# Performance work log

Hardware: AMD Instinct MI355X
Metric: run time of the kernel (lower is better)

Reference implementation:

```python
import jax, jax.numpy as jnp
import numpy as np

D_IN = 1024
D_OUT = 1024
NUM_HEADS = 16
HEAD_DIM = D_OUT // NUM_HEADS


def setup_inputs() -> dict:
    key = jax.random.key(0)
    k = jax.random.split(key, 6)
    s = 1.0 / np.sqrt(D_IN)
    return {
        "x": jax.random.normal(k[0], (2, 2048, D_IN), dtype=jnp.float32),
        "W_q": jax.random.uniform(k[1], (D_OUT, D_IN), jnp.float32, -s, s),
        "W_k": jax.random.uniform(k[2], (D_OUT, D_IN), jnp.float32, -s, s),
        "W_v": jax.random.uniform(k[3], (D_OUT, D_IN), jnp.float32, -s, s),
        "W_o": jax.random.uniform(k[4], (D_OUT, D_OUT), jnp.float32, -s, s),
        "b_o": jax.random.uniform(k[5], (D_OUT,), jnp.float32, -s, s),
    }


def reference(x, W_q, W_k, W_v, W_o, b_o):
    b, n, _ = x.shape
    h, hd = NUM_HEADS, HEAD_DIM
    # linear projections (torch Linear: x @ W.T), reshape to [b, h, n, hd]
    q = (x @ W_q.T).reshape(b, n, h, hd).transpose(0, 2, 1, 3)
    k = (x @ W_k.T).reshape(b, n, h, hd).transpose(0, 2, 1, 3)
    v = (x @ W_v.T).reshape(b, n, h, hd).transpose(0, 2, 1, 3)
    scores = jnp.einsum("bhqd,bhkd->bhqk", q, k) / np.sqrt(hd).astype(np.float32)
    causal = jnp.triu(jnp.full((n, n), -jnp.inf, dtype=scores.dtype), k=1)
    scores = scores + causal[None, None]
    weights = jax.nn.softmax(scores, axis=-1)  # dropout p=0.0 -> identity
    ctx = jnp.einsum("bhqk,bhkd->bhqd", weights, v)
    ctx = ctx.transpose(0, 2, 1, 3).reshape(b, n, h * hd)
    return ctx @ W_o.T + b_o
```

## Files before the change

### kernel.cpp

```cpp
#include <hip/hip_runtime.h>
#include <hip/hip_bf16.h>
#include <stdint.h>

typedef __attribute__((ext_vector_type(8)))  __bf16   bf16x8;
typedef __attribute__((ext_vector_type(4)))  float    f32x4;
typedef __attribute__((ext_vector_type(16))) float    f32x16;
typedef __attribute__((ext_vector_type(4)))  unsigned u32x4;
typedef __attribute__((ext_vector_type(2)))  unsigned u32x2;

#define BATCH  2
#define SEQ    2048
#define DMODEL 1024
#define NHEAD  16
#define HDIM   64
#define MTOT   (BATCH * SEQ)
#define MOFF   8.0f

__device__ __forceinline__ void gload_lds16(const void* g, void* l) {
  __builtin_amdgcn_global_load_lds(
      (const __attribute__((address_space(1))) unsigned int*)g,
      (__attribute__((address_space(3))) unsigned int*)(uintptr_t)l,
      16, 0, 0);
}

__device__ __forceinline__ unsigned pkbf(float a, float b) {
  unsigned lo = (unsigned)__builtin_bit_cast(unsigned short, (__bf16)a);
  unsigned hb = (unsigned)__builtin_bit_cast(unsigned short, (__bf16)b);
  return lo | (hb << 16);
}

__global__ void cast_all(const float* __restrict__ x,  const float* __restrict__ wq,
                         const float* __restrict__ wk, const float* __restrict__ wv,
                         const float* __restrict__ wo,
                         __bf16* __restrict__ xb,  __bf16* __restrict__ wqb,
                         __bf16* __restrict__ wkb, __bf16* __restrict__ wvb,
                         __bf16* __restrict__ wob)
{
  const float* in; __bf16* out; int n;
  switch (blockIdx.y) {
    case 0:  in = x;  out = xb;  n = MTOT * DMODEL;   break;
    case 1:  in = wq; out = wqb; n = DMODEL * DMODEL; break;
    case 2:  in = wk; out = wkb; n = DMODEL * DMODEL; break;
    case 3:  in = wv; out = wvb; n = DMODEL * DMODEL; break;
    default: in = wo; out = wob; n = DMODEL * DMODEL; break;
  }
  const int i = blockIdx.x * blockDim.x + threadIdx.x;
  const int stride = gridDim.x * blockDim.x;
  for (int idx = i; idx * 8 < n; idx += stride) {
    const float4 a = ((const float4*)in)[idx * 2];
    const float4 b = ((const float4*)in)[idx * 2 + 1];
    bf16x8 v = { (__bf16)a.x, (__bf16)a.y, (__bf16)a.z, (__bf16)a.w,
                 (__bf16)b.x, (__bf16)b.y, (__bf16)b.z, (__bf16)b.w };
    *(bf16x8*)(out + (size_t)idx * 8) = v;
  }
}

__device__ __forceinline__ void gemm_tile_128(const __bf16* __restrict__ A,
                                              const __bf16* __restrict__ W,
                                              int bm, int bn, int Kd,
                                              f32x4 (&acc)[4][4])
{
  __shared__ __align__(16) __bf16 As[128 * 32];
  __shared__ __align__(16) __bf16 Bs[128 * 32];
  const int tid  = threadIdx.x;
  const int wave = tid >> 6, lane = tid & 63;
  const int wr = wave >> 1, wc = wave & 1;
  const int fr = lane & 15, fq = lane >> 4;
  const int c0 = tid, c1 = tid + 256;
  const __bf16* gA0 = A + (size_t)(bm * 128 + (c0 >> 2)) * Kd + (c0 & 3) * 8;
  const __bf16* gA1 = A + (size_t)(bm * 128 + (c1 >> 2)) * Kd + (c1 & 3) * 8;
  const __bf16* gB0 = W + (size_t)(bn * 128 + (c0 >> 2)) * Kd + (c0 & 3) * 8;
  const __bf16* gB1 = W + (size_t)(bn * 128 + (c1 >> 2)) * Kd + (c1 & 3) * 8;

  for (int k0 = 0; k0 < Kd; k0 += 32) {
    gload_lds16(gA0 + k0, As + c0 * 8);
    gload_lds16(gB0 + k0, Bs + c0 * 8);
    gload_lds16(gA1 + k0, As + c1 * 8);
    gload_lds16(gB1 + k0, Bs + c1 * 8);
    __syncthreads();
    bf16x8 a[4], b[4];
#pragma unroll
    for (int m = 0; m < 4; ++m)
      a[m] = *(const bf16x8*)(As + (wr * 64 + m * 16 + fr) * 32 + fq * 8);
#pragma unroll
    for (int n = 0; n < 4; ++n)
      b[n] = *(const bf16x8*)(Bs + (wc * 64 + n * 16 + fr) * 32 + fq * 8);
#pragma unroll
    for (int m = 0; m < 4; ++m)
#pragma unroll
      for (int n = 0; n < 4; ++n)
        acc[m][n] = __builtin_amdgcn_mfma_f32_16x16x32_bf16(a[m], b[n], acc[m][n], 0, 0, 0);
    __syncthreads();
  }
}

__global__ __launch_bounds__(256)
void gemm_qkv(const __bf16* __restrict__ xb,
              const __bf16* __restrict__ Wq, const __bf16* __restrict__ Wk,
              const __bf16* __restrict__ Wv,
              __bf16* __restrict__ Qo, __bf16* __restrict__ Ko, __bf16* __restrict__ VTo,
              float qscale)
{
  const int z = blockIdx.z;
  const __bf16* A; const __bf16* W; __bf16* Ob; int bm, bn;
  if (z == 2)      { A = Wv; W = xb; Ob = VTo; bm = blockIdx.y; bn = blockIdx.x; }
  else if (z == 1) { A = xb; W = Wk; Ob = Ko;  bm = blockIdx.x; bn = blockIdx.y; }
  else             { A = xb; W = Wq; Ob = Qo;  bm = blockIdx.x; bn = blockIdx.y; }

  f32x4 acc[4][4] = {};
  gemm_tile_128(A, W, bm, bn, DMODEL, acc);

  const int lane = threadIdx.x & 63, wave = threadIdx.x >> 6;
  const int wr = wave >> 1, wc = wave & 1;
  const int fr = lane & 15, fq = lane >> 4;

  if (z == 0) {
#pragma unroll
    for (int m = 0; m < 4; ++m)
#pragma unroll
      for (int n = 0; n < 4; ++n) {
        const int col = bn * 128 + wc * 64 + n * 16 + fr;
#pragma unroll
        for (int j = 0; j < 4; ++j) {
          const int row = bm * 128 + wr * 64 + m * 16 + fq * 4 + j;
          Ob[(size_t)row * DMODEL + col] = (__bf16)(acc[m][n][j] * qscale);
        }
      }
  } else if (z == 1) {
#pragma unroll
    for (int m = 0; m < 4; ++m)
#pragma unroll
      for (int n = 0; n < 4; ++n) {
        const int f = bn * 128 + wc * 64 + n * 16 + fr;
        const int h = f >> 6;
        const int kc = (f >> 4) & 3, hi = (f >> 3) & 1, jj = f & 7;
#pragma unroll
        for (int j = 0; j < 4; ++j) {
          const int tkn = bm * 128 + wr * 64 + m * 16 + fq * 4 + j;
          const int bb = tkn >> 11, n2 = tkn & 2047;
          const int t32 = n2 >> 5, ln2 = n2 & 31;
          const size_t idx = (((((size_t)bb * 16 + h) * 64 + t32) * 4 + kc) * 64
                              + (ln2 + (hi << 5))) * 8 + jj;
          Ob[idx] = (__bf16)acc[m][n][j];
        }
      }
  } else {
#pragma unroll
    for (int m = 0; m < 4; ++m)
#pragma unroll
      for (int n = 0; n < 4; ++n) {
        const int tkn = bn * 128 + wc * 64 + n * 16 + fr;
        const int bb = tkn >> 11, n2 = tkn & 2047;
        const int t64 = n2 >> 6, w2 = n2 & 63;
        const int kc = w2 >> 4, hi = (w2 >> 3) & 1, jj = w2 & 7;
#pragma unroll
        for (int j = 0; j < 4; ++j) {
          const int f = bm * 128 + wr * 64 + m * 16 + fq * 4 + j;
          const int h = f >> 6, d = f & 63;
          const int db = d >> 5, ln2 = d & 31;
          const size_t idx = ((((((size_t)bb * 16 + h) * 32 + t64) * 2 + db) * 4 + kc) * 64
                              + (ln2 + (hi << 5))) * 8 + jj;
          Ob[idx] = (__bf16)acc[m][n][j];
        }
      }
  }
}

__global__ __launch_bounds__(256)
void gemm_out(const __bf16* __restrict__ A, const __bf16* __restrict__ W,
              float* __restrict__ OF, const float* __restrict__ bias)
{
  f32x4 acc[4][4] = {};
  gemm_tile_128(A, W, blockIdx.x, blockIdx.y, DMODEL, acc);

  const int lane = threadIdx.x & 63, wave = threadIdx.x >> 6;
  const int wr = wave >> 1, wc = wave & 1;
  const int fr = lane & 15, fq = lane >> 4;
#pragma unroll
  for (int m = 0; m < 4; ++m)
#pragma unroll
    for (int n = 0; n < 4; ++n) {
      const int col = blockIdx.y * 128 + wc * 64 + n * 16 + fr;
#pragma unroll
      for (int j = 0; j < 4; ++j) {
        const int row = blockIdx.x * 128 + wr * 64 + m * 16 + fq * 4 + j;
        OF[(size_t)row * DMODEL + col] = acc[m][n][j] + bias[col];
      }
    }
}


__device__ __forceinline__ void mask_tile(f32x16& sv0, f32x16& sv1,
                                          int kv0, int q0, int ln, int hi)
{
  const int qg = q0 + ln;
#pragma unroll
  for (int r = 0; r < 16; ++r) {
    const int kvo = kv0 + (r & 3) + 8 * (r >> 2) + 4 * hi;
    if (kvo > qg)      sv0[r] = -1e30f;
    if (kvo + 32 > qg) sv1[r] = -1e30f;
  }
}

__device__ __forceinline__ void pack_pf(const f32x16& sv0, const f32x16& sv1,
                                        bf16x8 (&pf)[4], int hi)
{
#pragma unroll
  for (int half = 0; half < 2; ++half) {
    const int r0 = half * 8;
    {
      unsigned pk01 = pkbf(sv0[r0 + 0], sv0[r0 + 1]);
      unsigned pk23 = pkbf(sv0[r0 + 2], sv0[r0 + 3]);
      unsigned pk45 = pkbf(sv0[r0 + 4], sv0[r0 + 5]);
      unsigned pk67 = pkbf(sv0[r0 + 6], sv0[r0 + 7]);
      unsigned x01 = (unsigned)__shfl_xor((int)pk01, 32, 64);
      unsigned x23 = (unsigned)__shfl_xor((int)pk23, 32, 64);
      unsigned x45 = (unsigned)__shfl_xor((int)pk45, 32, 64);
      unsigned x67 = (unsigned)__shfl_xor((int)pk67, 32, 64);
      u32x4 uw = { hi ? x45 : pk01, hi ? x67 : pk23,
                   hi ? pk45 : x01, hi ? pk67 : x23 };
      pf[half] = __builtin_bit_cast(bf16x8, uw);
    }
    {
      unsigned pk01 = pkbf(sv1[r0 + 0], sv1[r0 + 1]);
      unsigned pk23 = pkbf(sv1[r0 + 2], sv1[r0 + 3]);
      unsigned pk45 = pkbf(sv1[r0 + 4], sv1[r0 + 5]);
      unsigned pk67 = pkbf(sv1[r0 + 6], sv1[r0 + 7]);
      unsigned x01 = (unsigned)__shfl_xor((int)pk01, 32, 64);
      unsigned x23 = (unsigned)__shfl_xor((int)pk23, 32, 64);
      unsigned x45 = (unsigned)__shfl_xor((int)pk45, 32, 64);
      unsigned x67 = (unsigned)__shfl_xor((int)pk67, 32, 64);
      u32x4 uw = { hi ? x45 : pk01, hi ? x67 : pk23,
                   hi ? pk45 : x01, hi ? pk67 : x23 };
      pf[2 + half] = __builtin_bit_cast(bf16x8, uw);
    }
  }
}

__global__ __launch_bounds__(128, 3)
void attn_kernel(const __bf16* __restrict__ Qg, const __bf16* __restrict__ PK,
                 const __bf16* __restrict__ PV, __bf16* __restrict__ Og)
{
  __shared__ __align__(16) float Cs[2][32][68];
  __shared__ float Ls[2][2][32];

  const int tid  = threadIdx.x;
  const int p    = tid >> 6;
  const int lane = tid & 63;
  const int ln = lane & 31, hi = lane >> 5;
  const int bI = blockIdx.x;
  const int bh = bI & 31;
  const int qt = 63 - (bI >> 5);
  const int b = bh >> 4, h = bh & 15;

  const int q0 = qt * 32;
  const int nt = (qt >> 1) + 1;

  const __bf16* Kp = PK + (size_t)(b * 16 + h) * (64 * 4 * 64 * 8);
  const __bf16* Vp = PV + (size_t)(b * 16 + h) * (32 * 2 * 4 * 64 * 8);
  const __bf16* Qp = Qg + ((size_t)b * SEQ + q0 + ln) * DMODEL + h * HDIM + hi * 8;

  bf16x8 qf[4];
#pragma unroll
  for (int kc = 0; kc < 4; ++kc)
    qf[kc] = *(const bf16x8*)(Qp + kc * 16);

  f32x16 c0 = {}, c1 = {};
  float l = 0.f;

  for (int t = p; t < nt; t += 2) {
    const __bf16* kt = Kp + (size_t)t * 4096;
    const __bf16* vt = Vp + (size_t)t * 4096;

    bf16x8 kA[4], kB[4];
#pragma unroll
    for (int kc = 0; kc < 4; ++kc) {
      kA[kc] = *(const bf16x8*)(kt + (kc * 64 + lane) * 8);
      kB[kc] = *(const bf16x8*)(kt + 2048 + (kc * 64 + lane) * 8);
    }

    f32x16 s0 = {}, s1 = {};
    __builtin_amdgcn_s_setprio(1);
#pragma unroll
    for (int kc = 0; kc < 4; ++kc) {
      s0 = __builtin_amdgcn_mfma_f32_32x32x16_bf16(kA[kc], qf[kc], s0, 0, 0, 0);
      s1 = __builtin_amdgcn_mfma_f32_32x32x16_bf16(kB[kc], qf[kc], s1, 0, 0, 0);
    }
    __builtin_amdgcn_s_setprio(0);

    bf16x8 vt0[4], vt1[4];
#pragma unroll
    for (int kc = 0; kc < 4; ++kc) {
      vt0[kc] = *(const bf16x8*)(vt + (kc * 64 + lane) * 8);
      vt1[kc] = *(const bf16x8*)(vt + 2048 + (kc * 64 + lane) * 8);
    }

    if (t == nt - 1) mask_tile(s0, s1, t * 64, q0, ln, hi);

#pragma unroll
    for (int r = 0; r < 16; ++r) {
      s0[r] = __builtin_amdgcn_exp2f(s0[r] - MOFF);
      s1[r] = __builtin_amdgcn_exp2f(s1[r] - MOFF);
    }
    float s8[8];
#pragma unroll
    for (int r = 0; r < 8; ++r)
      s8[r] = (s0[r] + s0[r + 8]) + (s1[r] + s1[r + 8]);
#pragma unroll
    for (int r = 0; r < 4; ++r) s8[r] += s8[r + 4];
    l += (s8[0] + s8[1]) + (s8[2] + s8[3]);

    bf16x8 pf[4];
    pack_pf(s0, s1, pf, hi);

    __builtin_amdgcn_s_setprio(1);
#pragma unroll
    for (int kc = 0; kc < 4; ++kc)
      c0 = __builtin_amdgcn_mfma_f32_32x32x16_bf16(vt0[kc], pf[kc], c0, 0, 0, 0);
#pragma unroll
    for (int kc = 0; kc < 4; ++kc)
      c1 = __builtin_amdgcn_mfma_f32_32x32x16_bf16(vt1[kc], pf[kc], c1, 0, 0, 0);
    __builtin_amdgcn_s_setprio(0);
  }

#pragma unroll
  for (int g = 0; g < 4; ++g) {
    f32x4 v0 = { c0[4*g+0], c0[4*g+1], c0[4*g+2], c0[4*g+3] };
    f32x4 v1 = { c1[4*g+0], c1[4*g+1], c1[4*g+2], c1[4*g+3] };
    *(f32x4*)&Cs[p][ln][g * 8 + hi * 4]      = v0;
    *(f32x4*)&Cs[p][ln][32 + g * 8 + hi * 4] = v1;
  }
  Ls[p][hi][ln] = l;
  __syncthreads();

  const int qe = p * 16 + (lane >> 2);
  const int de = (lane & 3) * 16;
  const float lt = Ls[0][0][qe] + Ls[0][1][qe] + Ls[1][0][qe] + Ls[1][1][qe];
  const float inv = 1.0f / lt;
  f32x4 a0 = *(const f32x4*)&Cs[0][qe][de]      + *(const f32x4*)&Cs[1][qe][de];
  f32x4 a1 = *(const f32x4*)&Cs[0][qe][de + 4]  + *(const f32x4*)&Cs[1][qe][de + 4];
  f32x4 a2 = *(const f32x4*)&Cs[0][qe][de + 8]  + *(const f32x4*)&Cs[1][qe][de + 8];
  f32x4 a3 = *(const f32x4*)&Cs[0][qe][de + 12] + *(const f32x4*)&Cs[1][qe][de + 12];
  u32x4 w0 = { pkbf(a0[0] * inv, a0[1] * inv), pkbf(a0[2] * inv, a0[3] * inv),
               pkbf(a1[0] * inv, a1[1] * inv), pkbf(a1[2] * inv, a1[3] * inv) };
  u32x4 w1 = { pkbf(a2[0] * inv, a2[1] * inv), pkbf(a2[2] * inv, a2[3] * inv),
               pkbf(a3[0] * inv, a3[1] * inv), pkbf(a3[2] * inv, a3[3] * inv) };
  __bf16* Op = Og + ((size_t)b * SEQ + q0 + qe) * DMODEL + h * HDIM + de;
  *(u32x4*)(Op)     = w0;
  *(u32x4*)(Op + 8) = w1;
}

extern "C" void kernel_launch(void* const* d_in, const int* in_sizes, int n_in,
                              void* d_out, int out_size, void* d_ws, size_t ws_size,
                              hipStream_t stream) {
  (void)in_sizes; (void)n_in; (void)out_size; (void)ws_size;
  const float* x  = (const float*)d_in[0];
  const float* Wq = (const float*)d_in[1];
  const float* Wk = (const float*)d_in[2];
  const float* Wv = (const float*)d_in[3];
  const float* Wo = (const float*)d_in[4];
  const float* bo = (const float*)d_in[5];
  float* out = (float*)d_out;

  __bf16* ws  = (__bf16*)d_ws;
  __bf16* xb  = ws;
  __bf16* Wqb = xb  + (size_t)MTOT * DMODEL;
  __bf16* Wkb = Wqb + (size_t)DMODEL * DMODEL;
  __bf16* Wvb = Wkb + (size_t)DMODEL * DMODEL;
  __bf16* Wob = Wvb + (size_t)DMODEL * DMODEL;
  __bf16* Qb  = Wob + (size_t)DMODEL * DMODEL;
  __bf16* Kpk = Qb  + (size_t)MTOT * DMODEL;
  __bf16* Vpk = Kpk + (size_t)MTOT * DMODEL;
  __bf16* ctxb = xb;

  cast_all<<<dim3(256, 5), 256, 0, stream>>>(x, Wq, Wk, Wv, Wo,
                                             xb, Wqb, Wkb, Wvb, Wob);

  const float qscale = 0.125f * 1.4426950408889634f;
  gemm_qkv<<<dim3(32, 8, 3), 256, 0, stream>>>(xb, Wqb, Wkb, Wvb, Qb, Kpk, Vpk, qscale);

  attn_kernel<<<dim3(2048), 128, 0, stream>>>(Qb, Kpk, Vpk, ctxb);

  gemm_out<<<dim3(32, 8), 256, 0, stream>>>(ctxb, Wob, out, bo);
}
```

Baseline: 100.2 us.

## Use BK=64 tiles for QKV GEMM and split-K across wave groups in output GEMM

The QKV projection GEMM now stages 64-wide K slices in shared memory, halving the number of barrier pairs per tile. The output projection GEMM launches 512 threads per block, with two groups of four waves each covering half of K. Partial accumulators are combined through a shared-memory reduction before the bias is added and the result is written. This raises per-block parallelism for the 256-block output GEMM, which otherwise underfills the GPU, at the cost of more LDS (roughly 64KB for the reduction buffer) and an extra reduction pass.

```diff
diff --git a/kernel.cpp b/kernel.cpp
--- a/kernel.cpp
+++ b/kernel.cpp
@@ -55,41 +55,49 @@
   }
 }
 
-__device__ __forceinline__ void gemm_tile_128(const __bf16* __restrict__ A,
-                                              const __bf16* __restrict__ W,
-                                              int bm, int bn, int Kd,
-                                              f32x4 (&acc)[4][4])
-{
-  __shared__ __align__(16) __bf16 As[128 * 32];
-  __shared__ __align__(16) __bf16 Bs[128 * 32];
+__device__ __forceinline__ void gemm_tile_128_bk64(const __bf16* __restrict__ A,
+                                                   const __bf16* __restrict__ W,
+                                                   int bm, int bn, int Kd,
+                                                   f32x4 (&acc)[4][4])
+{
+  __shared__ __align__(16) __bf16 As[128 * 64];
+  __shared__ __align__(16) __bf16 Bs[128 * 64];
   const int tid  = threadIdx.x;
   const int wave = tid >> 6, lane = tid & 63;
   const int wr = wave >> 1, wc = wave & 1;
   const int fr = lane & 15, fq = lane >> 4;
-  const int c0 = tid, c1 = tid + 256;
-  const __bf16* gA0 = A + (size_t)(bm * 128 + (c0 >> 2)) * Kd + (c0 & 3) * 8;
-  const __bf16* gA1 = A + (size_t)(bm * 128 + (c1 >> 2)) * Kd + (c1 & 3) * 8;
-  const __bf16* gB0 = W + (size_t)(bn * 128 + (c0 >> 2)) * Kd + (c0 & 3) * 8;
-  const __bf16* gB1 = W + (size_t)(bn * 128 + (c1 >> 2)) * Kd + (c1 & 3) * 8;
-
-  for (int k0 = 0; k0 < Kd; k0 += 32) {
-    gload_lds16(gA0 + k0, As + c0 * 8);
-    gload_lds16(gB0 + k0, Bs + c0 * 8);
-    gload_lds16(gA1 + k0, As + c1 * 8);
-    gload_lds16(gB1 + k0, Bs + c1 * 8);
+
+  const __bf16* gA[4];
+  const __bf16* gB[4];
+#pragma unroll
+  for (int i = 0; i < 4; ++i) {
+    const int c = tid + 256 * i;
+    gA[i] = A + (size_t)(bm * 128 + (c >> 3)) * Kd + (c & 7) * 8;
+    gB[i] = W + (size_t)(bn * 128 + (c >> 3)) * Kd + (c & 7) * 8;
+  }
+
+  for (int k0 = 0; k0 < Kd; k0 += 64) {
+#pragma unroll
+    for (int i = 0; i < 4; ++i) {
+      gload_lds16(gA[i] + k0, As + (tid + 256 * i) * 8);
+      gload_lds16(gB[i] + k0, Bs + (tid + 256 * i) * 8);
+    }
     __syncthreads();
-    bf16x8 a[4], b[4];
-#pragma unroll
-    for (int m = 0; m < 4; ++m)
-      a[m] = *(const bf16x8*)(As + (wr * 64 + m * 16 + fr) * 32 + fq * 8);
-#pragma unroll
-    for (int n = 0; n < 4; ++n)
-      b[n] = *(const bf16x8*)(Bs + (wc * 64 + n * 16 + fr) * 32 + fq * 8);
-#pragma unroll
-    for (int m = 0; m < 4; ++m)
+#pragma unroll
+    for (int kc = 0; kc < 2; ++kc) {
+      bf16x8 a[4], b[4];
+#pragma unroll
+      for (int m = 0; m < 4; ++m)
+        a[m] = *(const bf16x8*)(As + (wr * 64 + m * 16 + fr) * 64 + kc * 32 + fq * 8);
 #pragma unroll
       for (int n = 0; n < 4; ++n)
-        acc[m][n] = __builtin_amdgcn_mfma_f32_16x16x32_bf16(a[m], b[n], acc[m][n], 0, 0, 0);
+        b[n] = *(const bf16x8*)(Bs + (wc * 64 + n * 16 + fr) * 64 + kc * 32 + fq * 8);
+#pragma unroll
+      for (int m = 0; m < 4; ++m)
+#pragma unroll
+        for (int n = 0; n < 4; ++n)
+          acc[m][n] = __builtin_amdgcn_mfma_f32_16x16x32_bf16(a[m], b[n], acc[m][n], 0, 0, 0);
+    }
     __syncthreads();
   }
 }
@@ -108,7 +116,7 @@
   else             { A = xb; W = Wq; Ob = Qo;  bm = blockIdx.x; bn = blockIdx.y; }
 
   f32x4 acc[4][4] = {};
-  gemm_tile_128(A, W, bm, bn, DMODEL, acc);
+  gemm_tile_128_bk64(A, W, bm, bn, DMODEL, acc);
 
   const int lane = threadIdx.x & 63, wave = threadIdx.x >> 6;
   const int wr = wave >> 1, wc = wave & 1;
@@ -166,27 +174,79 @@
   }
 }
 
-__global__ __launch_bounds__(256)
+__global__ __launch_bounds__(512)
 void gemm_out(const __bf16* __restrict__ A, const __bf16* __restrict__ W,
               float* __restrict__ OF, const float* __restrict__ bias)
 {
+  __shared__ __align__(16) __bf16 As[2][128 * 32];
+  __shared__ __align__(16) __bf16 Bs[2][128 * 32];
+  __shared__ __align__(16) float  Cred[4 * 16 * 64 * 4];
+
+  const int tid  = threadIdx.x;
+  const int wave = tid >> 6, lane = tid & 63;
+  const int g    = wave >> 2;
+  const int w4   = wave & 3;
+  const int wr = w4 >> 1, wc = w4 & 1;
+  const int fr = lane & 15, fq = lane >> 4;
+  const int bm = blockIdx.x, bn = blockIdx.y;
+
+  const int tid2 = tid & 255;
+  const int c0 = tid2, c1 = tid2 + 256;
+  const int kgo = g * 512;
+  const __bf16* gA0 = A + (size_t)(bm * 128 + (c0 >> 2)) * DMODEL + (c0 & 3) * 8 + kgo;
+  const __bf16* gA1 = A + (size_t)(bm * 128 + (c1 >> 2)) * DMODEL + (c1 & 3) * 8 + kgo;
+  const __bf16* gB0 = W + (size_t)(bn * 128 + (c0 >> 2)) * DMODEL + (c0 & 3) * 8 + kgo;
+  const __bf16* gB1 = W + (size_t)(bn * 128 + (c1 >> 2)) * DMODEL + (c1 & 3) * 8 + kgo;
+  __bf16* Asg = As[g];
+  __bf16* Bsg = Bs[g];
+
   f32x4 acc[4][4] = {};
-  gemm_tile_128(A, W, blockIdx.x, blockIdx.y, DMODEL, acc);
-
-  const int lane = threadIdx.x & 63, wave = threadIdx.x >> 6;
-  const int wr = wave >> 1, wc = wave & 1;
-  const int fr = lane & 15, fq = lane >> 4;
-#pragma unroll
-  for (int m = 0; m < 4; ++m)
-#pragma unroll
-    for (int n = 0; n < 4; ++n) {
-      const int col = blockIdx.y * 128 + wc * 64 + n * 16 + fr;
-#pragma unroll
-      for (int j = 0; j < 4; ++j) {
-        const int row = blockIdx.x * 128 + wr * 64 + m * 16 + fq * 4 + j;
-        OF[(size_t)row * DMODEL + col] = acc[m][n][j] + bias[col];
+
+  for (int k0 = 0; k0 < 512; k0 += 32) {
+    gload_lds16(gA0 + k0, Asg + c0 * 8);
+    gload_lds16(gB0 + k0, Bsg + c0 * 8);
+    gload_lds16(gA1 + k0, Asg + c1 * 8);
+    gload_lds16(gB1 + k0, Bsg + c1 * 8);
+    __syncthreads();
+    bf16x8 a[4], b[4];
+#pragma unroll
+    for (int m = 0; m < 4; ++m)
+      a[m] = *(const bf16x8*)(Asg + (wr * 64 + m * 16 + fr) * 32 + fq * 8);
+#pragma unroll
+    for (int n = 0; n < 4; ++n)
+      b[n] = *(const bf16x8*)(Bsg + (wc * 64 + n * 16 + fr) * 32 + fq * 8);
+#pragma unroll
+    for (int m = 0; m < 4; ++m)
+#pragma unroll
+      for (int n = 0; n < 4; ++n)
+        acc[m][n] = __builtin_amdgcn_mfma_f32_16x16x32_bf16(a[m], b[n], acc[m][n], 0, 0, 0);
+    __syncthreads();
+  }
+
+  if (g == 1) {
+#pragma unroll
+    for (int m = 0; m < 4; ++m)
+#pragma unroll
+      for (int n = 0; n < 4; ++n)
+        *(f32x4*)&Cred[(((w4 * 16) + m * 4 + n) * 64 + lane) * 4] = acc[m][n];
+  }
+  __syncthreads();
+
+  if (g == 0) {
+#pragma unroll
+    for (int m = 0; m < 4; ++m)
+#pragma unroll
+      for (int n = 0; n < 4; ++n) {
+        const f32x4 part = *(const f32x4*)&Cred[(((w4 * 16) + m * 4 + n) * 64 + lane) * 4];
+        const int col = bn * 128 + wc * 64 + n * 16 + fr;
+        const float bv = bias[col];
+#pragma unroll
+        for (int j = 0; j < 4; ++j) {
+          const int row = bm * 128 + wr * 64 + m * 16 + fq * 4 + j;
+          OF[(size_t)row * DMODEL + col] = acc[m][n][j] + part[j] + bv;
+        }
       }
-    }
+  }
 }
 
 
@@ -381,5 +441,5 @@
 
   attn_kernel<<<dim3(2048), 128, 0, stream>>>(Qb, Kpk, Vpk, ctxb);
 
-  gemm_out<<<dim3(32, 8), 256, 0, stream>>>(ctxb, Wob, out, bo);
-}
+  gemm_out<<<dim3(32, 8), 512, 0, stream>>>(ctxb, Wob, out, bo);
+}
```

Result: slower. 113.9 us (+13.7%).
